# Optimization experiments

Hardware: AMD Instinct MI355X
Metric: run time of the kernel (lower is better)

Reference implementation:

```python
import jax, jax.numpy as jnp
import numpy as np

B, V, J, NS, NE = 2048, 5023, 5, 300, 100
PARENTS = np.array([-1, 0, 1, 1, 1])  # FLAME kintree: neck<-global, jaw/eyes<-neck


def _rodrigues(rvecs):
    """Axis-angle [..., 3] -> rotation matrices [..., 3, 3] (smplx convention)."""
    angle = jnp.linalg.norm(rvecs + 1e-8, axis=-1, keepdims=True)  # [...,1]
    axis = rvecs / angle
    rx, ry, rz = axis[..., 0], axis[..., 1], axis[..., 2]
    z = jnp.zeros_like(rx)
    K = jnp.stack([z, -rz, ry, rz, z, -rx, -ry, rx, z], axis=-1)
    K = K.reshape(rvecs.shape[:-1] + (3, 3))
    s = jnp.sin(angle)[..., None]
    c = jnp.cos(angle)[..., None]
    eye = jnp.eye(3, dtype=rvecs.dtype)
    return eye + s * K + (1.0 - c) * jnp.matmul(K, K)


def setup_inputs() -> dict:
    key = jax.random.key(0)
    ks = jax.random.split(key, 12)
    jr = jax.random.uniform(ks[9], (J, V), dtype=jnp.float32)
    jr = jr / jnp.sum(jr, axis=1, keepdims=True)
    w = jax.random.uniform(ks[10], (V, J), dtype=jnp.float32)
    w = w / jnp.sum(w, axis=1, keepdims=True)  # skinning weights sum to 1
    return {
        'shape': 0.1 * jax.random.normal(ks[0], (B, NS), dtype=jnp.float32),
        'expr': 0.1 * jax.random.normal(ks[1], (B, NE), dtype=jnp.float32),
        'global_pose': 0.1 * jax.random.normal(ks[2], (B, 3), dtype=jnp.float32),
        'neck_pose': 0.1 * jax.random.normal(ks[3], (B, 3), dtype=jnp.float32),
        'jaw_pose': 0.1 * jax.random.normal(ks[4], (B, 3), dtype=jnp.float32),
        'eye_pose': 0.1 * jax.random.normal(ks[5], (B, 6), dtype=jnp.float32),
        'v_template': jax.random.normal(ks[6], (V, 3), dtype=jnp.float32),
        'shape_dirs': 0.01 * jax.random.normal(ks[7], (V, 3, NS + NE), dtype=jnp.float32),
        'pose_dirs': 0.01 * jax.random.normal(ks[8], (36, V * 3), dtype=jnp.float32),
        'J_regressor': jr,
        'lbs_weights': w,
        'parents': jnp.asarray(PARENTS, dtype=jnp.int32),
    }


def reference(shape, expr, global_pose, neck_pose, jaw_pose, eye_pose,
              v_template, shape_dirs, pose_dirs, J_regressor, lbs_weights, parents):
    b = shape.shape[0]
    betas = jnp.concatenate([shape, expr], axis=1)                       # [B, NS+NE]
    full_pose = jnp.concatenate([global_pose, neck_pose, jaw_pose, eye_pose], axis=1)  # [B, 15]

    # shape/expression blendshapes
    v_shaped = v_template[None] + jnp.einsum('bl,vkl->bvk', betas, shape_dirs)  # [B,V,3]
    joints = jnp.einsum('jv,bvk->bjk', J_regressor, v_shaped)                   # [B,J,3]

    # pose -> rotation matrices, pose blendshapes
    rot_mats = _rodrigues(full_pose.reshape(b, J, 3))                           # [B,J,3,3]
    eye3 = jnp.eye(3, dtype=rot_mats.dtype)
    pose_feature = (rot_mats[:, 1:] - eye3).reshape(b, (J - 1) * 9)             # [B,36]
    v_posed = v_shaped + (pose_feature @ pose_dirs).reshape(b, V, 3)

    # rigid transforms along kinematic tree (J=5, unrolled Python loop)
    par = PARENTS
    rel_joints = jnp.concatenate([joints[:, :1], joints[:, 1:] - joints[:, par[1:]]], axis=1)
    tm = jnp.concatenate([rot_mats, rel_joints[..., None]], axis=-1)            # [B,J,3,4]
    bottom = jnp.broadcast_to(jnp.array([0., 0., 0., 1.], tm.dtype), (b, J, 1, 4))
    tm4 = jnp.concatenate([tm, bottom], axis=-2)                                # [B,J,4,4]
    chain = [tm4[:, 0]]
    for i in range(1, J):
        chain.append(jnp.matmul(chain[int(par[i])], tm4[:, i]))
    transforms = jnp.stack(chain, axis=1)                                       # [B,J,4,4]

    joints_hom = jnp.concatenate([joints, jnp.zeros((b, J, 1), joints.dtype)], axis=-1)
    tj = jnp.einsum('bjxy,bjy->bjx', transforms, joints_hom)
    A = transforms.at[..., :, 3].add(-tj)  # relative transforms w.r.t. rest joints

    # linear blend skinning
    T = jnp.einsum('vj,bjxy->bvxy', lbs_weights, A)                             # [B,V,4,4]
    v_hom = jnp.concatenate([v_posed, jnp.ones((b, V, 1), v_posed.dtype)], axis=-1)
    verts = jnp.einsum('bvxy,bvy->bvx', T, v_hom)[..., :3]                      # [B,V,3]
    return verts, rot_mats
```

## Files before the change

### kernel.cpp

```cpp
#include <hip/hip_runtime.h>
#include <hip/hip_bf16.h>
#include <math.h>

#define B_    2048
#define V_    5023
#define N3    15069
#define VOFF  30861312

#define BM    256
#define BN    96
#define NKC   14
#define NBX   157
#define NBY   8

#define OFF_CBT    0
#define OFF_SDTT   458752
#define OFF_JSP    0
#define OFF_JS     3834880
#define OFF_JT     3840880
#define OFF_A      3840896

#define NCH 512
#define CHV 10

typedef __attribute__((ext_vector_type(8))) short short8;
typedef __attribute__((ext_vector_type(4))) float f32x4;

typedef __attribute__((address_space(1))) const void gvoid_t;
typedef __attribute__((address_space(3))) void lvoid_t;
#define GLDS16(g, l) __builtin_amdgcn_global_load_lds((gvoid_t*)(g), (lvoid_t*)(l), 16, 0, 0)

__global__ void __launch_bounds__(512) k_js(
    const float* __restrict__ Jreg, const float* __restrict__ SD,
    const float* __restrict__ VT, float* __restrict__ ws) {
    int ch = blockIdx.x;
    int v0 = ch * CHV;
    int t = threadIdx.x;
    __shared__ float jw[5][CHV];
    for (int s = t; s < 5 * CHV; s += 512) {
        int j = s / CHV, vi = s % CHV;
        int v = v0 + vi;
        jw[j][vi] = (v < V_) ? Jreg[j * V_ + v] : 0.f;
    }
    __syncthreads();
    int nv = min(V_ - v0, CHV);
    if (t < 400) {
        float acc[15];
        #pragma unroll
        for (int i = 0; i < 15; ++i) acc[i] = 0.f;
        for (int vi = 0; vi < nv; ++vi) {
            int v = v0 + vi;
            float s0 = SD[(v * 3 + 0) * 400 + t];
            float s1 = SD[(v * 3 + 1) * 400 + t];
            float s2 = SD[(v * 3 + 2) * 400 + t];
            #pragma unroll
            for (int j = 0; j < 5; ++j) {
                float jr = jw[j][vi];
                acc[j * 3 + 0] += jr * s0;
                acc[j * 3 + 1] += jr * s1;
                acc[j * 3 + 2] += jr * s2;
            }
        }
        #pragma unroll
        for (int i = 0; i < 15; ++i)
            ws[OFF_JSP + (i * 400 + t) * NCH + ch] = acc[i];
    } else if (t >= 448 && t < 463) {
        int jk = t - 448, j = jk / 3, k = jk % 3;
        float a = 0.f;
        for (int vi = 0; vi < nv; ++vi)
            a += jw[j][vi] * VT[(v0 + vi) * 3 + k];
        ws[OFF_JSP + (6000 + jk) * NCH + ch] = a;
    }
}

__global__ void k_js_reduce(float* __restrict__ ws) {
    int r = blockIdx.x * 256 + threadIdx.x;
    if (r >= 6016) return;
    const float4* p = (const float4*)&ws[OFF_JSP + r * NCH];
    float4 s4 = {0.f, 0.f, 0.f, 0.f};
    for (int i = 0; i < NCH / 4; ++i) {
        float4 v = p[i];
        s4.x += v.x; s4.y += v.y; s4.z += v.z; s4.w += v.w;
    }
    float s = s4.x + s4.y + s4.z + s4.w;
    if (r < 6000) ws[OFF_JS + r] = s;
    else if (r < 6015) ws[OFF_JT + (r - 6000)] = s;
}

__global__ void k_sdt_tiled(const float* __restrict__ SD, const float* __restrict__ PD,
                            float* __restrict__ ws) {
    int id = blockIdx.x * 256 + threadIdx.x;
    if (id >= NBX * NKC * 6 * 64) return;
    int lane = id & 63;
    int t = id >> 6;
    int j = t % 6; t /= 6;
    int kc = t % NKC, bx = t / NKC;
    int n = bx * 96 + j * 16 + (lane & 15);
    int k0 = kc * 32 + (lane >> 4) * 8;
    union { __hip_bfloat16 h[8]; uint4 u; } pk;
    if (n < N3 && k0 + 8 <= 400) {
        const float4* s = (const float4*)&SD[n * 400 + k0];
        float4 a = s[0], b = s[1];
        pk.h[0] = __float2bfloat16(a.x); pk.h[1] = __float2bfloat16(a.y);
        pk.h[2] = __float2bfloat16(a.z); pk.h[3] = __float2bfloat16(a.w);
        pk.h[4] = __float2bfloat16(b.x); pk.h[5] = __float2bfloat16(b.y);
        pk.h[6] = __float2bfloat16(b.z); pk.h[7] = __float2bfloat16(b.w);
    } else {
        #pragma unroll
        for (int e = 0; e < 8; ++e) {
            int k = k0 + e;
            float v = 0.f;
            if (n < N3) {
                if (k < 400) v = SD[n * 400 + k];
                else if (k < 436) v = PD[(k - 400) * N3 + n];
            }
            pk.h[e] = __float2bfloat16(v);
        }
    }
    ((uint4*)((char*)ws + OFF_SDTT * 4))[id] = pk.u;
}

__global__ void k_cbt_tiled(const float* __restrict__ sh, const float* __restrict__ ex,
                            float* __restrict__ ws) {
    int id = blockIdx.x * 256 + threadIdx.x;
    if (id >= NBY * NKC * 16 * 64) return;
    int lane = id & 63;
    int t = id >> 6;
    int mf = t & 15; t >>= 4;
    int kc = t % NKC, by = t / NKC;
    int b = by * BM + mf * 16 + (lane & 15);
    int k0 = kc * 32 + (lane >> 4) * 8;
    union { __hip_bfloat16 h[8]; uint4 u; } pk;
    #pragma unroll
    for (int e = 0; e < 8; ++e) {
        int k = k0 + e;
        float v = 0.f;
        if (k < 300) v = sh[b * 300 + k];
        else if (k < 400) v = ex[b * 100 + (k - 300)];
        pk.h[e] = __float2bfloat16(v);
    }
    ((uint4*)ws)[id] = pk.u;
}

__device__ __forceinline__ int cbt_idx(int b, int k) {
    int by = b >> 8, mf = (b & 255) >> 4, cr = b & 15;
    int kc = k >> 5, kg = (k & 31) >> 3, e = k & 7;
    return (((by * NKC + kc) * 16 + mf) * 64 + kg * 16 + cr) * 8 + e;
}

__device__ __forceinline__ void rodrigues(float rx, float ry, float rz, float* R) {
    float ax = rx + 1e-8f, ay = ry + 1e-8f, az = rz + 1e-8f;
    float ang = sqrtf(ax * ax + ay * ay + az * az);
    float inv = 1.f / ang;
    float ux = rx * inv, uy = ry * inv, uz = rz * inv;
    float s = sinf(ang), c = cosf(ang), m = 1.f - c;
    R[0] = 1.f + m * (-uz * uz - uy * uy);
    R[1] = -s * uz + m * ux * uy;
    R[2] =  s * uy + m * ux * uz;
    R[3] =  s * uz + m * ux * uy;
    R[4] = 1.f + m * (-uz * uz - ux * ux);
    R[5] = -s * ux + m * uy * uz;
    R[6] = -s * uy + m * ux * uz;
    R[7] =  s * ux + m * uy * uz;
    R[8] = 1.f + m * (-uy * uy - ux * ux);
}

__global__ void __launch_bounds__(256) k_batch(
    const float* __restrict__ gp, const float* __restrict__ npo,
    const float* __restrict__ jp, const float* __restrict__ ep,
    const float* __restrict__ sh, const float* __restrict__ ex,
    float* __restrict__ out, float* __restrict__ ws) {
    __shared__ float js_l[6000];
    __shared__ float jtp[4][64][15];
    int tid = threadIdx.x;
    int w = tid >> 6, lane = tid & 63;
    int b = blockIdx.x * 64 + lane;
    for (int s = tid; s < 6000; s += 256) js_l[s] = ws[OFF_JS + s];
    __syncthreads();
    float p15[15];
    #pragma unroll
    for (int q = 0; q < 15; ++q) p15[q] = 0.f;
    for (int i = 0; i < 100; ++i) {
        int k = 100 * w + i;
        float cl = (w < 3) ? sh[b * 300 + k] : ex[b * 100 + i];
        #pragma unroll
        for (int q = 0; q < 15; ++q) p15[q] += js_l[q * 400 + k] * cl;
    }
    #pragma unroll
    for (int q = 0; q < 15; ++q) jtp[w][lane][q] = p15[q];
    __syncthreads();
    if (w != 0) return;

    float jt[15];
    #pragma unroll
    for (int q = 0; q < 15; ++q)
        jt[q] = ws[OFF_JT + q] + jtp[0][lane][q] + jtp[1][lane][q]
              + jtp[2][lane][q] + jtp[3][lane][q];

    float R[5][9];
    rodrigues(gp[b * 3], gp[b * 3 + 1], gp[b * 3 + 2], R[0]);
    rodrigues(npo[b * 3], npo[b * 3 + 1], npo[b * 3 + 2], R[1]);
    rodrigues(jp[b * 3], jp[b * 3 + 1], jp[b * 3 + 2], R[2]);
    rodrigues(ep[b * 6], ep[b * 6 + 1], ep[b * 6 + 2], R[3]);
    rodrigues(ep[b * 6 + 3], ep[b * 6 + 4], ep[b * 6 + 5], R[4]);
    for (int j = 0; j < 5; ++j)
        for (int i = 0; i < 9; ++i)
            out[VOFF + b * 45 + j * 9 + i] = R[j][i];
    __hip_bfloat16* cb = (__hip_bfloat16*)ws;
    for (int j = 1; j < 5; ++j)
        for (int i = 0; i < 9; ++i)
            cb[cbt_idx(b, 400 + (j - 1) * 9 + i)] =
                __float2bfloat16(R[j][i] - ((i == 0 || i == 4 || i == 8) ? 1.f : 0.f));

    const int par[5] = {0, 0, 1, 1, 1};
    float rel[5][3];
    for (int k = 0; k < 3; ++k) rel[0][k] = jt[k];
    for (int j = 1; j < 5; ++j)
        for (int k = 0; k < 3; ++k) rel[j][k] = jt[j * 3 + k] - jt[par[j] * 3 + k];
    float Rc[5][9], tc[5][3];
    for (int i = 0; i < 9; ++i) Rc[0][i] = R[0][i];
    for (int k = 0; k < 3; ++k) tc[0][k] = rel[0][k];
    for (int j = 1; j < 5; ++j) {
        int p = par[j];
        for (int r = 0; r < 3; ++r) {
            for (int c2 = 0; c2 < 3; ++c2) {
                float s = 0.f;
                for (int m = 0; m < 3; ++m) s += Rc[p][r * 3 + m] * R[j][m * 3 + c2];
                Rc[j][r * 3 + c2] = s;
            }
            float tv = 0.f;
            for (int m = 0; m < 3; ++m) tv += Rc[p][r * 3 + m] * rel[j][m];
            tc[j][r] = tv + tc[p][r];
        }
    }
    for (int j = 0; j < 5; ++j)
        for (int r = 0; r < 3; ++r) {
            float tj = 0.f;
            for (int m = 0; m < 3; ++m) tj += Rc[j][r * 3 + m] * jt[j * 3 + m];
            ws[OFF_A + b * 60 + j * 12 + r * 4 + 0] = Rc[j][r * 3 + 0];
            ws[OFF_A + b * 60 + j * 12 + r * 4 + 1] = Rc[j][r * 3 + 1];
            ws[OFF_A + b * 60 + j * 12 + r * 4 + 2] = Rc[j][r * 3 + 2];
            ws[OFF_A + b * 60 + j * 12 + r * 4 + 3] = tc[j][r] - tj;
        }
}

__global__ void __launch_bounds__(256, 3) k_gemm_lbs(
    const float* __restrict__ VT, const float* __restrict__ W,
    const float* __restrict__ ws, float* __restrict__ out) {
    __shared__ __align__(16) char smem[45056];

    const char* cbt  = (const char*)ws;
    const char* sdtt = (const char*)ws + (size_t)OFF_SDTT * 4;
    const float* Amat = ws + OFF_A;

    int flat = blockIdx.x;
    int nid = (flat & 7) * 157 + (flat >> 3);
    int bx = nid >> 3, by = nid & 7;
    int n0 = bx * BN, b0 = by * BM, v0 = bx * 32;

    int tid = threadIdx.x;
    int w = tid >> 6, lane = tid & 63;

    const char* Aglb = cbt + (size_t)(by * NKC) * 16384;
    const char* Bglb = sdtt + (size_t)(bx * NKC) * 6144;

    auto stage = [&](int kc, int p) {
        char* lA = smem + p * 22528;
        char* lB = lA + 16384;
        const char* ga = Aglb + (size_t)kc * 16384;
        const char* gb = Bglb + (size_t)kc * 6144;
        #pragma unroll
        for (int c = 0; c < 4; ++c) {
            int ch = 4 * w + c;
            GLDS16(ga + ch * 1024 + lane * 16, lA + ch * 1024);
        }
        if (w < 3) {
            #pragma unroll
            for (int c = 0; c < 2; ++c) {
                int ch = 2 * w + c;
                GLDS16(gb + ch * 1024 + lane * 16, lB + ch * 1024);
            }
        }
    };

    stage(0, 0);
    stage(1, 1);

    f32x4 acc[4][6];
    #pragma unroll
    for (int m = 0; m < 4; ++m)
        #pragma unroll
        for (int j = 0; j < 6; ++j) acc[m][j] = (f32x4){0.f, 0.f, 0.f, 0.f};

    for (int kc = 0; kc < NKC; ++kc) {
        int p = kc & 1;
        if (kc < NKC - 1) {
            if (w < 3) asm volatile("s_waitcnt vmcnt(6)" ::: "memory");
            else       asm volatile("s_waitcnt vmcnt(4)" ::: "memory");
        } else {
            asm volatile("s_waitcnt vmcnt(0)" ::: "memory");
        }
        __builtin_amdgcn_s_barrier();
        const char* lA = smem + p * 22528;
        const char* lB = lA + 16384;
        short8 af[4];
        #pragma unroll
        for (int m = 0; m < 4; ++m)
            af[m] = *(const short8*)(lA + (4 * w + m) * 1024 + lane * 16);
        #pragma unroll
        for (int j = 0; j < 6; ++j) {
            short8 bf = *(const short8*)(lB + j * 1024 + lane * 16);
            #pragma unroll
            for (int m = 0; m < 4; ++m)
                acc[m][j] = __builtin_amdgcn_mfma_f32_16x16x32_bf16(af[m], bf, acc[m][j], 0, 0, 0);
        }
        __builtin_amdgcn_s_barrier();
        if (kc + 2 < NKC) stage(kc + 2, p);
    }

    float vt6[6];
    #pragma unroll
    for (int j = 0; j < 6; ++j) {
        int n = n0 + 16 * j + (lane & 15);
        vt6[j] = (n < N3) ? VT[n] : 0.f;
    }
    int vl = tid & 31, v = v0 + vl;
    bool vok = v < V_;
    float w5[5] = {0.f, 0.f, 0.f, 0.f, 0.f};
    if (vok)
        #pragma unroll
        for (int j = 0; j < 5; ++j) w5[j] = W[v * 5 + j];

    float* Am = (float*)smem;
    float* Ps = (float*)(smem + 15872);

    #pragma unroll
    for (int h = 0; h < 4; ++h) {
        const float4* Ag = (const float4*)&Amat[(b0 + 64 * h) * 60];
        for (int s = tid; s < 960; s += 256)
            ((float4*)Am)[s] = Ag[s];
        if (w == h) {
            #pragma unroll
            for (int j = 0; j < 6; ++j) {
                int col = 16 * j + (lane & 15);
                #pragma unroll
                for (int m = 0; m < 4; ++m) {
                    int lrow = 16 * m + 4 * (lane >> 4);
                    #pragma unroll
                    for (int i = 0; i < 4; ++i)
                        Ps[(lrow + i) * 98 + col] = acc[m][j][i] + vt6[j];
                }
            }
        }
        __syncthreads();
        #pragma unroll 2
        for (int q = 0; q < 8; ++q) {
            int bl = (tid >> 5) + 8 * q;
            float px = Ps[bl * 98 + 3 * vl + 0];
            float py = Ps[bl * 98 + 3 * vl + 1];
            float pz = Ps[bl * 98 + 3 * vl + 2];
            if (vok) {
                const float4* Aq = (const float4*)&Am[bl * 60];
                float4 t0 = {0,0,0,0}, t1 = {0,0,0,0}, t2 = {0,0,0,0};
                #pragma unroll
                for (int j = 0; j < 5; ++j) {
                    float wj = w5[j];
                    float4 a0 = Aq[j * 3 + 0], a1 = Aq[j * 3 + 1], a2 = Aq[j * 3 + 2];
                    t0.x += wj * a0.x; t0.y += wj * a0.y; t0.z += wj * a0.z; t0.w += wj * a0.w;
                    t1.x += wj * a1.x; t1.y += wj * a1.y; t1.z += wj * a1.z; t1.w += wj * a1.w;
                    t2.x += wj * a2.x; t2.y += wj * a2.y; t2.z += wj * a2.z; t2.w += wj * a2.w;
                }
                int b = b0 + 64 * h + bl;
                int ob = b * N3 + v * 3;
                out[ob + 0] = t0.x * px + t0.y * py + t0.z * pz + t0.w;
                out[ob + 1] = t1.x * px + t1.y * py + t1.z * pz + t1.w;
                out[ob + 2] = t2.x * px + t2.y * py + t2.z * pz + t2.w;
            }
        }
        __syncthreads();
    }
}

extern "C" void kernel_launch(void* const* d_in, const int* in_sizes, int n_in,
                              void* d_out, int out_size, void* d_ws, size_t ws_size,
                              hipStream_t stream) {
    const float* shape = (const float*)d_in[0];
    const float* expr  = (const float*)d_in[1];
    const float* gpose = (const float*)d_in[2];
    const float* npose = (const float*)d_in[3];
    const float* jpose = (const float*)d_in[4];
    const float* epose = (const float*)d_in[5];
    const float* vt    = (const float*)d_in[6];
    const float* sd    = (const float*)d_in[7];
    const float* pd    = (const float*)d_in[8];
    const float* jreg  = (const float*)d_in[9];
    const float* w     = (const float*)d_in[10];
    float* out = (float*)d_out;
    float* ws  = (float*)d_ws;

    k_js<<<NCH, 512, 0, stream>>>(jreg, sd, vt, ws);
    k_js_reduce<<<24, 256, 0, stream>>>(ws);
    k_sdt_tiled<<<(NBX * NKC * 6 * 64 + 255) / 256, 256, 0, stream>>>(sd, pd, ws);
    k_cbt_tiled<<<(NBY * NKC * 16 * 64 + 255) / 256, 256, 0, stream>>>(shape, expr, ws);
    k_batch<<<32, 256, 0, stream>>>(gpose, npose, jpose, epose, shape, expr, out, ws);
    k_gemm_lbs<<<NBX * NBY, 256, 0, stream>>>(vt, w, ws, out);
}
```

Before: 142.0 us.

## Stage shape/pose-dir bf16 repack through LDS and transpose js partial layout

The shape_dirs/pose_dirs bf16 repack kernel now loads a 16-row strip into shared memory with coalesced reads, then writes the MFMA-tiled fragments from LDS. This replaces per-thread strided float4 loads and the uncoalesced pose_dirs gather. The joint-shape partial buffer is also transposed to a chunk-major layout, so k_js writes and k_js_reduce reads are coalesced across threads instead of strided by NCH. The cost is extra LDS use, a block barrier, and a serial scalar reduce loop per thread.

```diff
diff --git a/kernel.cpp b/kernel.cpp
--- a/kernel.cpp
+++ b/kernel.cpp
@@ -63,61 +63,56 @@
         }
         #pragma unroll
         for (int i = 0; i < 15; ++i)
-            ws[OFF_JSP + (i * 400 + t) * NCH + ch] = acc[i];
+            ws[OFF_JSP + ch * 6016 + i * 400 + t] = acc[i];
     } else if (t >= 448 && t < 463) {
         int jk = t - 448, j = jk / 3, k = jk % 3;
         float a = 0.f;
         for (int vi = 0; vi < nv; ++vi)
             a += jw[j][vi] * VT[(v0 + vi) * 3 + k];
-        ws[OFF_JSP + (6000 + jk) * NCH + ch] = a;
+        ws[OFF_JSP + ch * 6016 + 6000 + jk] = a;
     }
 }
 
 __global__ void k_js_reduce(float* __restrict__ ws) {
     int r = blockIdx.x * 256 + threadIdx.x;
     if (r >= 6016) return;
-    const float4* p = (const float4*)&ws[OFF_JSP + r * NCH];
-    float4 s4 = {0.f, 0.f, 0.f, 0.f};
-    for (int i = 0; i < NCH / 4; ++i) {
-        float4 v = p[i];
-        s4.x += v.x; s4.y += v.y; s4.z += v.z; s4.w += v.w;
-    }
-    float s = s4.x + s4.y + s4.z + s4.w;
+    float s = 0.f;
+    for (int ch = 0; ch < NCH; ++ch) s += ws[OFF_JSP + ch * 6016 + r];
     if (r < 6000) ws[OFF_JS + r] = s;
     else if (r < 6015) ws[OFF_JT + (r - 6000)] = s;
 }
 
-__global__ void k_sdt_tiled(const float* __restrict__ SD, const float* __restrict__ PD,
-                            float* __restrict__ ws) {
-    int id = blockIdx.x * 256 + threadIdx.x;
-    if (id >= NBX * NKC * 6 * 64) return;
-    int lane = id & 63;
-    int t = id >> 6;
-    int j = t % 6; t /= 6;
-    int kc = t % NKC, bx = t / NKC;
-    int n = bx * 96 + j * 16 + (lane & 15);
-    int k0 = kc * 32 + (lane >> 4) * 8;
-    union { __hip_bfloat16 h[8]; uint4 u; } pk;
-    if (n < N3 && k0 + 8 <= 400) {
-        const float4* s = (const float4*)&SD[n * 400 + k0];
-        float4 a = s[0], b = s[1];
-        pk.h[0] = __float2bfloat16(a.x); pk.h[1] = __float2bfloat16(a.y);
-        pk.h[2] = __float2bfloat16(a.z); pk.h[3] = __float2bfloat16(a.w);
-        pk.h[4] = __float2bfloat16(b.x); pk.h[5] = __float2bfloat16(b.y);
-        pk.h[6] = __float2bfloat16(b.z); pk.h[7] = __float2bfloat16(b.w);
-    } else {
-        #pragma unroll
-        for (int e = 0; e < 8; ++e) {
-            int k = k0 + e;
-            float v = 0.f;
-            if (n < N3) {
-                if (k < 400) v = SD[n * 400 + k];
-                else if (k < 436) v = PD[(k - 400) * N3 + n];
-            }
-            pk.h[e] = __float2bfloat16(v);
-        }
-    }
-    ((uint4*)((char*)ws + OFF_SDTT * 4))[id] = pk.u;
+__global__ void __launch_bounds__(256) k_sdt_lds(
+    const float* __restrict__ SD, const float* __restrict__ PD,
+    float* __restrict__ ws) {
+    __shared__ __hip_bfloat16 lb[16][456];
+    int bid = blockIdx.x;
+    int bx = bid / 6, jl = bid % 6;
+    int n0 = bx * 96 + jl * 16;
+    int tid = threadIdx.x;
+    for (int s = tid; s < 16 * 400; s += 256) {
+        int r = s / 400, c = s % 400;
+        int n = n0 + r;
+        lb[r][c] = __float2bfloat16((n < N3) ? SD[n * 400 + c] : 0.f);
+    }
+    for (int s = tid; s < 36 * 16; s += 256) {
+        int p = s / 16, r = s % 16;
+        int n = n0 + r;
+        lb[r][400 + p] = __float2bfloat16((n < N3) ? PD[p * N3 + n] : 0.f);
+    }
+    for (int s = tid; s < 12 * 16; s += 256) {
+        int c = s / 16, r = s % 16;
+        lb[r][436 + c] = __float2bfloat16(0.f);
+    }
+    __syncthreads();
+    uint4* sdtt = (uint4*)((char*)ws + (size_t)OFF_SDTT * 4);
+    for (int s = tid; s < NKC * 64; s += 256) {
+        int kc = s >> 6, lane = s & 63;
+        int r = lane & 15;
+        int k0 = kc * 32 + (lane >> 4) * 8;
+        uint4 val = *(const uint4*)&lb[r][k0];
+        sdtt[((size_t)(bx * NKC + kc) * 6 + jl) * 64 + lane] = val;
+    }
 }
 
 __global__ void k_cbt_tiled(const float* __restrict__ sh, const float* __restrict__ ex,
@@ -400,7 +395,7 @@
 
     k_js<<<NCH, 512, 0, stream>>>(jreg, sd, vt, ws);
     k_js_reduce<<<24, 256, 0, stream>>>(ws);
-    k_sdt_tiled<<<(NBX * NKC * 6 * 64 + 255) / 256, 256, 0, stream>>>(sd, pd, ws);
+    k_sdt_lds<<<NBX * 6, 256, 0, stream>>>(sd, pd, ws);
     k_cbt_tiled<<<(NBY * NKC * 16 * 64 + 255) / 256, 256, 0, stream>>>(shape, expr, ws);
     k_batch<<<32, 256, 0, stream>>>(gpose, npose, jpose, epose, shape, expr, out, ws);
     k_gemm_lbs<<<NBX * NBY, 256, 0, stream>>>(vt, w, ws, out);
```

New measurement: 124.5 us (median of 2 runs). 1.14x faster.
